# Performance work log

Measured on AMD Instinct MI355X. Metric: run time of the kernel, lower is better.

Reference implementation:

```python
import jax, jax.numpy as jnp
import numpy as np

H = 256  # hidden_dim


def _mlp(x, w1, b1, w2, b2):
    # Linear -> ReLU -> (Dropout=identity in eval) -> Linear
    return jax.nn.relu(x @ w1 + b1) @ w2 + b2


def setup_inputs() -> dict:
    key = jax.random.key(0)
    ks = jax.random.split(key, 9)
    bsz, seq = 32, 4096
    s = 1.0 / np.sqrt(2 * H)
    inp = {
        "h": jax.random.normal(ks[0], (bsz, seq, H), dtype=jnp.float32),
        "mask": jnp.ones((bsz, seq), dtype=jnp.float32),
        "ew1": jax.random.uniform(ks[1], (2 * H, H), minval=-s, maxval=s),
        "eb1": jax.random.uniform(ks[2], (H,), minval=-s, maxval=s),
        "ew2": jax.random.uniform(ks[3], (H, H), minval=-s, maxval=s),
        "eb2": jax.random.uniform(ks[4], (H,), minval=-s, maxval=s),
        "nw1": jax.random.uniform(ks[5], (2 * H, H), minval=-s, maxval=s),
        "nb1": jax.random.uniform(ks[6], (H,), minval=-s, maxval=s),
        "nw2": jax.random.uniform(ks[7], (H, H), minval=-s, maxval=s),
        "nb2": jax.random.uniform(ks[8], (H,), minval=-s, maxval=s),
    }
    return inp


def reference(h, mask, ew1, eb1, ew2, eb2, nw1, nb1, nw2, nb2):
    left = h[:, :-1, :]   # [B, S-1, H]
    right = h[:, 1:, :]   # [B, S-1, H]
    m_lr = _mlp(jnp.concatenate([left, right], axis=-1), ew1, eb1, ew2, eb2)
    m_rl = _mlp(jnp.concatenate([right, left], axis=-1), ew1, eb1, ew2, eb2)
    # shifted scatter-add: agg[:,1:] += m_lr ; agg[:,:-1] += m_rl
    zcol = jnp.zeros_like(h[:, :1, :])
    agg = jnp.concatenate([zcol, m_lr], axis=1) + jnp.concatenate([m_rl, zcol], axis=1)
    updated = _mlp(jnp.concatenate([h, agg], axis=-1), nw1, nb1, nw2, nb2)
    updated = updated * mask[:, :, None]
    return h + updated
```

## Files before the change

### kernel.cpp

```cpp
#include <hip/hip_runtime.h>
#include <hip/hip_bf16.h>

typedef __bf16 bf16_t;
typedef bf16_t bf16x8 __attribute__((ext_vector_type(8)));
typedef bf16_t bf16x4 __attribute__((ext_vector_type(4)));
typedef float f32x4 __attribute__((ext_vector_type(4)));

#define SEQ 4096
#define BSZ 32
#define T_TOK 96
#define TILES 43
#define PROWS 98
#define LSTR 264
#define NPANEL (PROWS * LSTR)

#define OFF_X 0
#define OFF_A NPANEL
#define OFF_B (2 * NPANEL)
#define SMEM_ELEMS (3 * NPANEL)
#define SMEM_BYTES (SMEM_ELEMS * 2)

#define W1F 0
#define NAF 131072
#define WBF 196608
#define N2F 262144
#define B2N 327680

#define BAR() asm volatile("s_waitcnt lgkmcnt(0)\n\ts_barrier" ::: "memory")

__global__ void wprep(const float* __restrict__ ew1, const float* __restrict__ nw1,
                      const float* __restrict__ nw2, bf16_t* __restrict__ wsw) {
    int idx = blockIdx.x * 256 + threadIdx.x;
    int region, rel, outbase;
    if (idx < 131072)      { region = 0; rel = idx;          outbase = W1F; }
    else if (idx < 196608) { region = 1; rel = idx - 131072; outbase = NAF; }
    else                   { region = 2; rel = idx - 196608; outbase = N2F; }
    int f = rel >> 9, o = rel & 511;
    int l = o >> 3, e = o & 7;
    int r = l & 15, kg = l >> 4;
    int nt = f >> 3, ks = f & 7;
    int k = ks * 32 + kg * 8 + e;
    int n = nt * 16 + r;
    float v;
    if (region == 0)
        v = (nt < 16) ? ew1[k * 256 + n] : ew1[(256 + k) * 256 + (n - 256)];
    else if (region == 1)
        v = nw1[k * 256 + n];
    else
        v = nw2[k * 256 + n];
    wsw[outbase + rel] = (bf16_t)v;
}

__global__ void wprep2(const float* __restrict__ ew2, const float* __restrict__ eb2,
                       const float* __restrict__ nw1, bf16_t* __restrict__ wsw) {
    int k = blockIdx.x;
    int n = threadIdx.x;
    if (k < 256) {
        float acc = 0.f;
        for (int j = 0; j < 256; ++j)
            acc += ew2[k * 256 + j] * nw1[(256 + j) * 256 + n];
        int ks = k >> 5, kg = (k >> 3) & 3, e = k & 7;
        int nt = n >> 4, r = n & 15;
        wsw[WBF + ((nt * 8 + ks) << 9) + ((kg * 16 + r) << 3) + e] = (bf16_t)acc;
    } else {
        float acc = 0.f;
        for (int j = 0; j < 256; ++j)
            acc += eb2[j] * nw1[(256 + j) * 256 + n];
        ((float*)(wsw + B2N))[n] = acc;
    }
}

__launch_bounds__(512, 2)
__global__ void gnl_kernel(const float* __restrict__ h, const float* __restrict__ mask,
                           const float* __restrict__ eb1, const float* __restrict__ nb1,
                           const float* __restrict__ nb2,
                           const bf16_t* __restrict__ wsw, float* __restrict__ out) {
    extern __shared__ bf16_t sm[];

    const int tid   = threadIdx.x;
    const int lane  = tid & 63;
    const int w     = tid >> 6;
    const int batch = blockIdx.x / TILES;
    const int tile  = blockIdx.x % TILES;
    const int t0    = tile * T_TOK;
    const long baseTok = (long)batch * SEQ;

    const int c   = lane & 15;
    const int kg  = lane >> 4;
    const int crb = kg << 2;
    const int n0a = w * 16;
    const int n0b = (w + 8) * 16;

    auto loadw = [&](bf16x8 (&f)[8], int base, int nt) {
#pragma unroll
        for (int ks = 0; ks < 8; ++ks)
            f[ks] = *(const bf16x8*)(wsw + base + ((nt * 8 + ks) << 9) + (lane << 3));
    };
    auto loada = [&](bf16x8 (&f)[8], int poff, int rbase) {
        const bf16_t* p = sm + poff + (rbase + c) * LSTR + (kg << 3);
#pragma unroll
        for (int ks = 0; ks < 8; ++ks) f[ks] = *(const bf16x8*)(p + (ks << 5));
    };
    auto mfma2 = [&](bf16x8 (&f)[8], bf16x8 (&wa)[8], bf16x8 (&wb)[8],
                     f32x4& a0, f32x4& a1) {
        __builtin_amdgcn_s_setprio(1);
#pragma unroll
        for (int ks = 0; ks < 8; ++ks) {
            a0 = __builtin_amdgcn_mfma_f32_16x16x32_bf16(wa[ks], f[ks], a0, 0, 0, 0);
            a1 = __builtin_amdgcn_mfma_f32_16x16x32_bf16(wb[ks], f[ks], a1, 0, 0, 0);
        }
        __builtin_amdgcn_s_setprio(0);
    };

    bf16x8 wa0[8], wb0[8];
    loadw(wa0, W1F, w);
    loadw(wb0, W1F, w + 8);

#pragma unroll
    for (int it = 0; it < 7; ++it) {
        int cc = tid + it * 512;
        if (cc < PROWS * 32) {
            int r = cc >> 5;
            int fc = (cc & 31) << 3;
            int t = t0 - 1 + r;
            bf16x8 v;
            if (t >= 0 && t < SEQ) {
                const float* src = h + (((long)(baseTok + t)) << 8) + fc;
                float4 x0 = ((const float4*)src)[0];
                float4 x1 = ((const float4*)src)[1];
                v[0] = (bf16_t)x0.x; v[1] = (bf16_t)x0.y;
                v[2] = (bf16_t)x0.z; v[3] = (bf16_t)x0.w;
                v[4] = (bf16_t)x1.x; v[5] = (bf16_t)x1.y;
                v[6] = (bf16_t)x1.z; v[7] = (bf16_t)x1.w;
            } else {
#pragma unroll
                for (int q = 0; q < 8; ++q) v[q] = (bf16_t)0.0f;
            }
            *(bf16x8*)(sm + OFF_X + r * LSTR + fc) = v;
        }
    }
    BAR();

#pragma unroll
    for (int p = 0; p < 2; ++p) {
        bf16x8 wa[8], wb[8];
        if (p == 0) {
#pragma unroll
            for (int ks = 0; ks < 8; ++ks) { wa[ks] = wa0[ks]; wb[ks] = wb0[ks]; }
        } else {
            loadw(wa, W1F, w + 16);
            loadw(wb, W1F, w + 24);
        }
        int poff = p ? OFF_B : OFF_A;
        bf16x8 fA[8], fB[8];
        loada(fA, OFF_X, 0);
#pragma unroll
        for (int mt = 0; mt < 7; ++mt) {
            bf16x8 (&cur)[8] = (mt & 1) ? fB : fA;
            bf16x8 (&nxt)[8] = (mt & 1) ? fA : fB;
            if (mt < 6) loada(nxt, OFF_X, (mt + 1) * 16);
            f32x4 aA = {0.f, 0.f, 0.f, 0.f}, aB = {0.f, 0.f, 0.f, 0.f};
            mfma2(cur, wa, wb, aA, aB);
            int row = mt * 16 + c;
            if (row < PROWS) {
                bf16x4 pA, pB;
#pragma unroll
                for (int q = 0; q < 4; ++q) { pA[q] = (bf16_t)aA[q]; pB[q] = (bf16_t)aB[q]; }
                *(bf16x4*)(sm + poff + row * LSTR + n0a + crb) = pA;
                *(bf16x4*)(sm + poff + row * LSTR + n0b + crb) = pB;
            }
        }
    }

    bf16x8 na[8], nb8[8], wba[8], wbb[8];
    loadw(na, NAF, w);
    loadw(nb8, NAF, w + 8);
    loadw(wba, WBF, w);
    loadw(wbb, WBF, w + 8);
    BAR();

    bf16x8 svr[6];
#pragma unroll
    for (int it = 0; it < 6; ++it) {
        int cc = tid + it * 512;
        int i = cc >> 5;
        int fc = (cc & 31) << 3;
        float bl = (t0 + i >= 1) ? 1.f : 0.f;
        float br = (t0 + i <= SEQ - 2) ? 1.f : 0.f;
        bf16x8 aL = *(const bf16x8*)(sm + OFF_A + i * LSTR + fc);
        bf16x8 aR = *(const bf16x8*)(sm + OFF_A + (i + 2) * LSTR + fc);
        bf16x8 bC = *(const bf16x8*)(sm + OFF_B + (i + 1) * LSTR + fc);
        float4 b1a = *(const float4*)(eb1 + fc);
        float4 b1b = *(const float4*)(eb1 + fc + 4);
        bf16x8 sv;
#pragma unroll
        for (int q = 0; q < 8; ++q) {
            float b1f = (q < 4) ? ((const float*)&b1a)[q] : ((const float*)&b1b)[q - 4];
            float x = (float)bC[q] + b1f;
            float l = fmaxf((float)aL[q] + x, 0.f) * bl;
            float r = fmaxf((float)aR[q] + x, 0.f) * br;
            sv[q] = (bf16_t)(l + r);
        }
        svr[it] = sv;
    }
    BAR();
#pragma unroll
    for (int it = 0; it < 6; ++it) {
        int cc = tid + it * 512;
        int i = cc >> 5;
        int fc = (cc & 31) << 3;
        *(bf16x8*)(sm + OFF_B + i * LSTR + fc) = svr[it];
    }
    BAR();

    {
        float4 n1a = *(const float4*)(nb1 + n0a + crb);
        float4 n1b = *(const float4*)(nb1 + n0b + crb);
        const float* b2n = (const float*)(wsw + B2N);
        float4 c2a = *(const float4*)(b2n + n0a + crb);
        float4 c2b = *(const float4*)(b2n + n0b + crb);
        bf16x8 fX[8], fS[8];
#pragma unroll
        for (int tm = 0; tm < 6; ++tm) {
            loada(fX, OFF_X, 1 + tm * 16);
            loada(fS, OFF_B, tm * 16);
            f32x4 a0 = {0.f, 0.f, 0.f, 0.f}, a1 = {0.f, 0.f, 0.f, 0.f};
            mfma2(fX, na, nb8, a0, a1);
            mfma2(fS, wba, wbb, a0, a1);
            int row = tm * 16 + c;
            int t = t0 + row;
            float cnt = ((t >= 1) ? 1.f : 0.f) + ((t <= SEQ - 2) ? 1.f : 0.f);
            bf16x4 p0, p1;
#pragma unroll
            for (int q = 0; q < 4; ++q) {
                p0[q] = (bf16_t)fmaxf(a0[q] + ((const float*)&n1a)[q] + cnt * ((const float*)&c2a)[q], 0.f);
                p1[q] = (bf16_t)fmaxf(a1[q] + ((const float*)&n1b)[q] + cnt * ((const float*)&c2b)[q], 0.f);
            }
            *(bf16x4*)(sm + OFF_A + row * LSTR + n0a + crb) = p0;
            *(bf16x4*)(sm + OFF_A + row * LSTR + n0b + crb) = p1;
        }
    }
    bf16x8 n2a[8], n2b[8];
    loadw(n2a, N2F, w);
    loadw(n2b, N2F, w + 8);
    BAR();

    {
        float4 v2a = *(const float4*)(nb2 + n0a + crb);
        float4 v2b = *(const float4*)(nb2 + n0b + crb);
        bf16x8 fA[8], fB[8];
        loada(fA, OFF_A, 0);
#pragma unroll
        for (int tm = 0; tm < 6; ++tm) {
            int row = tm * 16 + c;
            int tok = t0 + row;
            int tokc = (tok < SEQ) ? tok : (SEQ - 1);
            long t = baseTok + tokc;
            float m = mask[t];
            bf16x8 (&cur)[8] = (tm & 1) ? fB : fA;
            bf16x8 (&nxt)[8] = (tm & 1) ? fA : fB;
            if (tm < 5) loada(nxt, OFF_A, (tm + 1) * 16);
            f32x4 a0 = {0.f, 0.f, 0.f, 0.f}, a1 = {0.f, 0.f, 0.f, 0.f};
            mfma2(cur, n2a, n2b, a0, a1);
            int rrow = row + 1;
            bf16x4 r0 = *(const bf16x4*)(sm + OFF_X + rrow * LSTR + n0a + crb);
            bf16x4 r1 = *(const bf16x4*)(sm + OFF_X + rrow * LSTR + n0b + crb);
            if (tok < SEQ) {
                long g0 = (t << 8) + n0a + crb;
                long g1 = (t << 8) + n0b + crb;
                float4 o0, o1;
                o0.x = (float)r0[0] + m * (a0[0] + v2a.x);
                o0.y = (float)r0[1] + m * (a0[1] + v2a.y);
                o0.z = (float)r0[2] + m * (a0[2] + v2a.z);
                o0.w = (float)r0[3] + m * (a0[3] + v2a.w);
                o1.x = (float)r1[0] + m * (a1[0] + v2b.x);
                o1.y = (float)r1[1] + m * (a1[1] + v2b.y);
                o1.z = (float)r1[2] + m * (a1[2] + v2b.z);
                o1.w = (float)r1[3] + m * (a1[3] + v2b.w);
                *(float4*)(out + g0) = o0;
                *(float4*)(out + g1) = o1;
            }
        }
    }
}

extern "C" void kernel_launch(void* const* d_in, const int* in_sizes, int n_in,
                              void* d_out, int out_size, void* d_ws, size_t ws_size,
                              hipStream_t stream) {
    const float* h    = (const float*)d_in[0];
    const float* mask = (const float*)d_in[1];
    const float* ew1  = (const float*)d_in[2];
    const float* eb1  = (const float*)d_in[3];
    const float* ew2  = (const float*)d_in[4];
    const float* eb2  = (const float*)d_in[5];
    const float* nw1  = (const float*)d_in[6];
    const float* nb1  = (const float*)d_in[7];
    const float* nw2  = (const float*)d_in[8];
    const float* nb2  = (const float*)d_in[9];
    float* out   = (float*)d_out;
    bf16_t* wsw  = (bf16_t*)d_ws;

    wprep<<<1024, 256, 0, stream>>>(ew1, nw1, nw2, wsw);
    wprep2<<<257, 256, 0, stream>>>(ew2, eb2, nw1, wsw);

    hipFuncSetAttribute(reinterpret_cast<const void*>(gnl_kernel),
                        hipFuncAttributeMaxDynamicSharedMemorySize, SMEM_BYTES);

    gnl_kernel<<<BSZ * TILES, 512, SMEM_BYTES, stream>>>(
        h, mask, eb1, nb1, nb2, wsw, out);
}
```

Measured before the change: 146.8 us.

## Shrink token tile, software-pipeline input load, split node GEMM to cut registers

Reduces the per-block token tile from 96 to 86 (48 tiles per batch), so LDS panels get smaller and more blocks can be resident, with loada clamping rows for the partial last MMA tile. Global loads of h are double-buffered so the next stage's fetch is issued before the current stage is converted and stored. The aggregate computation now writes in place, dropping a barrier and the staging registers. The node layer-1 GEMM is split into two passes with the partial sum kept in LDS, so only one weight set is live at a time. The cost is extra LDS traffic and bf16 rounding of the intermediate partial sum, plus some wasted MMA work on padded rows.

```diff
diff --git a/kernel.cpp b/kernel.cpp
--- a/kernel.cpp
+++ b/kernel.cpp
@@ -8,9 +8,9 @@
 
 #define SEQ 4096
 #define BSZ 32
-#define T_TOK 96
-#define TILES 43
-#define PROWS 98
+#define T_TOK 86
+#define TILES 48
+#define PROWS 88
 #define LSTR 264
 #define NPANEL (PROWS * LSTR)
 
@@ -97,7 +97,9 @@
             f[ks] = *(const bf16x8*)(wsw + base + ((nt * 8 + ks) << 9) + (lane << 3));
     };
     auto loada = [&](bf16x8 (&f)[8], int poff, int rbase) {
-        const bf16_t* p = sm + poff + (rbase + c) * LSTR + (kg << 3);
+        int rr = rbase + c;
+        rr = (rr < PROWS) ? rr : (PROWS - 1);
+        const bf16_t* p = sm + poff + rr * LSTR + (kg << 3);
 #pragma unroll
         for (int ks = 0; ks < 8; ++ks) f[ks] = *(const bf16x8*)(p + (ks << 5));
     };
@@ -116,27 +118,46 @@
     loadw(wa0, W1F, w);
     loadw(wb0, W1F, w + 8);
 
-#pragma unroll
-    for (int it = 0; it < 7; ++it) {
-        int cc = tid + it * 512;
-        if (cc < PROWS * 32) {
-            int r = cc >> 5;
-            int fc = (cc & 31) << 3;
-            int t = t0 - 1 + r;
-            bf16x8 v;
-            if (t >= 0 && t < SEQ) {
-                const float* src = h + (((long)(baseTok + t)) << 8) + fc;
-                float4 x0 = ((const float4*)src)[0];
-                float4 x1 = ((const float4*)src)[1];
-                v[0] = (bf16_t)x0.x; v[1] = (bf16_t)x0.y;
-                v[2] = (bf16_t)x0.z; v[3] = (bf16_t)x0.w;
-                v[4] = (bf16_t)x1.x; v[5] = (bf16_t)x1.y;
-                v[6] = (bf16_t)x1.z; v[7] = (bf16_t)x1.w;
-            } else {
-#pragma unroll
-                for (int q = 0; q < 8; ++q) v[q] = (bf16_t)0.0f;
-            }
-            *(bf16x8*)(sm + OFF_X + r * LSTR + fc) = v;
+    {
+        float4 pa0, pa1, pb0, pb1;
+        auto issue_stage = [&](int it, float4& q0, float4& q1) {
+            int cc = tid + it * 512;
+            if (cc < PROWS * 32) {
+                int r = cc >> 5, fc = (cc & 31) << 3;
+                int t = t0 - 1 + r;
+                int tc = (t < 0) ? 0 : ((t > SEQ - 1) ? SEQ - 1 : t);
+                const float* src = h + (((long)(baseTok + tc)) << 8) + fc;
+                q0 = ((const float4*)src)[0];
+                q1 = ((const float4*)src)[1];
+            }
+        };
+        auto write_stage = [&](int it, const float4& q0, const float4& q1) {
+            int cc = tid + it * 512;
+            if (cc < PROWS * 32) {
+                int r = cc >> 5, fc = (cc & 31) << 3;
+                int t = t0 - 1 + r;
+                bf16x8 v;
+                if (t >= 0 && t < SEQ) {
+                    v[0] = (bf16_t)q0.x; v[1] = (bf16_t)q0.y;
+                    v[2] = (bf16_t)q0.z; v[3] = (bf16_t)q0.w;
+                    v[4] = (bf16_t)q1.x; v[5] = (bf16_t)q1.y;
+                    v[6] = (bf16_t)q1.z; v[7] = (bf16_t)q1.w;
+                } else {
+#pragma unroll
+                    for (int q = 0; q < 8; ++q) v[q] = (bf16_t)0.0f;
+                }
+                *(bf16x8*)(sm + OFF_X + r * LSTR + fc) = v;
+            }
+        };
+        issue_stage(0, pa0, pa1);
+#pragma unroll
+        for (int it = 0; it < 6; ++it) {
+            if (it < 5) {
+                if (it & 1) issue_stage(it + 1, pa0, pa1);
+                else        issue_stage(it + 1, pb0, pb1);
+            }
+            if (it & 1) write_stage(it, pb0, pb1);
+            else        write_stage(it, pa0, pa1);
         }
     }
     BAR();
@@ -155,10 +176,10 @@
         bf16x8 fA[8], fB[8];
         loada(fA, OFF_X, 0);
 #pragma unroll
-        for (int mt = 0; mt < 7; ++mt) {
+        for (int mt = 0; mt < 6; ++mt) {
             bf16x8 (&cur)[8] = (mt & 1) ? fB : fA;
             bf16x8 (&nxt)[8] = (mt & 1) ? fA : fB;
-            if (mt < 6) loada(nxt, OFF_X, (mt + 1) * 16);
+            if (mt < 5) loada(nxt, OFF_X, (mt + 1) * 16);
             f32x4 aA = {0.f, 0.f, 0.f, 0.f}, aB = {0.f, 0.f, 0.f, 0.f};
             mfma2(cur, wa, wb, aA, aB);
             int row = mt * 16 + c;
@@ -172,72 +193,86 @@
         }
     }
 
-    bf16x8 na[8], nb8[8], wba[8], wbb[8];
+    bf16x8 na[8], nb8[8];
     loadw(na, NAF, w);
     loadw(nb8, NAF, w + 8);
-    loadw(wba, WBF, w);
-    loadw(wbb, WBF, w + 8);
     BAR();
 
-    bf16x8 svr[6];
 #pragma unroll
     for (int it = 0; it < 6; ++it) {
         int cc = tid + it * 512;
-        int i = cc >> 5;
-        int fc = (cc & 31) << 3;
-        float bl = (t0 + i >= 1) ? 1.f : 0.f;
-        float br = (t0 + i <= SEQ - 2) ? 1.f : 0.f;
-        bf16x8 aL = *(const bf16x8*)(sm + OFF_A + i * LSTR + fc);
-        bf16x8 aR = *(const bf16x8*)(sm + OFF_A + (i + 2) * LSTR + fc);
-        bf16x8 bC = *(const bf16x8*)(sm + OFF_B + (i + 1) * LSTR + fc);
-        float4 b1a = *(const float4*)(eb1 + fc);
-        float4 b1b = *(const float4*)(eb1 + fc + 4);
-        bf16x8 sv;
-#pragma unroll
-        for (int q = 0; q < 8; ++q) {
-            float b1f = (q < 4) ? ((const float*)&b1a)[q] : ((const float*)&b1b)[q - 4];
-            float x = (float)bC[q] + b1f;
-            float l = fmaxf((float)aL[q] + x, 0.f) * bl;
-            float r = fmaxf((float)aR[q] + x, 0.f) * br;
-            sv[q] = (bf16_t)(l + r);
-        }
-        svr[it] = sv;
+        if (cc < T_TOK * 32) {
+            int i = cc >> 5;
+            int fc = (cc & 31) << 3;
+            float bl = (t0 + i >= 1) ? 1.f : 0.f;
+            float br = (t0 + i <= SEQ - 2) ? 1.f : 0.f;
+            bf16x8 aL = *(const bf16x8*)(sm + OFF_A + i * LSTR + fc);
+            bf16x8 aR = *(const bf16x8*)(sm + OFF_A + (i + 2) * LSTR + fc);
+            bf16x8 bC = *(const bf16x8*)(sm + OFF_B + (i + 1) * LSTR + fc);
+            float4 b1a = *(const float4*)(eb1 + fc);
+            float4 b1b = *(const float4*)(eb1 + fc + 4);
+            bf16x8 sv;
+#pragma unroll
+            for (int q = 0; q < 8; ++q) {
+                float b1f = (q < 4) ? ((const float*)&b1a)[q] : ((const float*)&b1b)[q - 4];
+                float x = (float)bC[q] + b1f;
+                float l = fmaxf((float)aL[q] + x, 0.f) * bl;
+                float r = fmaxf((float)aR[q] + x, 0.f) * br;
+                sv[q] = (bf16_t)(l + r);
+            }
+            *(bf16x8*)(sm + OFF_B + (i + 1) * LSTR + fc) = sv;
+        }
     }
     BAR();
-#pragma unroll
-    for (int it = 0; it < 6; ++it) {
-        int cc = tid + it * 512;
-        int i = cc >> 5;
-        int fc = (cc & 31) << 3;
-        *(bf16x8*)(sm + OFF_B + i * LSTR + fc) = svr[it];
-    }
-    BAR();
 
     {
+        bf16x8 fX[8];
+#pragma unroll
+        for (int tm = 0; tm < 6; ++tm) {
+            loada(fX, OFF_X, 1 + tm * 16);
+            f32x4 a0 = {0.f, 0.f, 0.f, 0.f}, a1 = {0.f, 0.f, 0.f, 0.f};
+            mfma2(fX, na, nb8, a0, a1);
+            int row = tm * 16 + c;
+            if (row < T_TOK) {
+                bf16x4 p0, p1;
+#pragma unroll
+                for (int q = 0; q < 4; ++q) { p0[q] = (bf16_t)a0[q]; p1[q] = (bf16_t)a1[q]; }
+                *(bf16x4*)(sm + OFF_A + row * LSTR + n0a + crb) = p0;
+                *(bf16x4*)(sm + OFF_A + row * LSTR + n0b + crb) = p1;
+            }
+        }
+    }
+
+    {
+        bf16x8 wba[8], wbb[8];
+        loadw(wba, WBF, w);
+        loadw(wbb, WBF, w + 8);
         float4 n1a = *(const float4*)(nb1 + n0a + crb);
         float4 n1b = *(const float4*)(nb1 + n0b + crb);
         const float* b2n = (const float*)(wsw + B2N);
         float4 c2a = *(const float4*)(b2n + n0a + crb);
         float4 c2b = *(const float4*)(b2n + n0b + crb);
-        bf16x8 fX[8], fS[8];
+        bf16x8 fS[8];
 #pragma unroll
         for (int tm = 0; tm < 6; ++tm) {
-            loada(fX, OFF_X, 1 + tm * 16);
-            loada(fS, OFF_B, tm * 16);
+            loada(fS, OFF_B, 1 + tm * 16);
             f32x4 a0 = {0.f, 0.f, 0.f, 0.f}, a1 = {0.f, 0.f, 0.f, 0.f};
-            mfma2(fX, na, nb8, a0, a1);
             mfma2(fS, wba, wbb, a0, a1);
             int row = tm * 16 + c;
-            int t = t0 + row;
-            float cnt = ((t >= 1) ? 1.f : 0.f) + ((t <= SEQ - 2) ? 1.f : 0.f);
-            bf16x4 p0, p1;
-#pragma unroll
-            for (int q = 0; q < 4; ++q) {
-                p0[q] = (bf16_t)fmaxf(a0[q] + ((const float*)&n1a)[q] + cnt * ((const float*)&c2a)[q], 0.f);
-                p1[q] = (bf16_t)fmaxf(a1[q] + ((const float*)&n1b)[q] + cnt * ((const float*)&c2b)[q], 0.f);
-            }
-            *(bf16x4*)(sm + OFF_A + row * LSTR + n0a + crb) = p0;
-            *(bf16x4*)(sm + OFF_A + row * LSTR + n0b + crb) = p1;
+            if (row < T_TOK) {
+                bf16x4 q0 = *(const bf16x4*)(sm + OFF_A + row * LSTR + n0a + crb);
+                bf16x4 q1 = *(const bf16x4*)(sm + OFF_A + row * LSTR + n0b + crb);
+                int t = t0 + row;
+                float cnt = ((t >= 1) ? 1.f : 0.f) + ((t <= SEQ - 2) ? 1.f : 0.f);
+                bf16x4 p0, p1;
+#pragma unroll
+                for (int q = 0; q < 4; ++q) {
+                    p0[q] = (bf16_t)fmaxf(a0[q] + (float)q0[q] + ((const float*)&n1a)[q] + cnt * ((const float*)&c2a)[q], 0.f);
+                    p1[q] = (bf16_t)fmaxf(a1[q] + (float)q1[q] + ((const float*)&n1b)[q] + cnt * ((const float*)&c2b)[q], 0.f);
+                }
+                *(bf16x4*)(sm + OFF_A + row * LSTR + n0a + crb) = p0;
+                *(bf16x4*)(sm + OFF_A + row * LSTR + n0b + crb) = p1;
+            }
         }
     }
     bf16x8 n2a[8], n2b[8];
@@ -263,9 +298,10 @@
             f32x4 a0 = {0.f, 0.f, 0.f, 0.f}, a1 = {0.f, 0.f, 0.f, 0.f};
             mfma2(cur, n2a, n2b, a0, a1);
             int rrow = row + 1;
+            rrow = (rrow < PROWS) ? rrow : (PROWS - 1);
             bf16x4 r0 = *(const bf16x4*)(sm + OFF_X + rrow * LSTR + n0a + crb);
             bf16x4 r1 = *(const bf16x4*)(sm + OFF_X + rrow * LSTR + n0b + crb);
-            if (tok < SEQ) {
+            if (row < T_TOK && tok < SEQ) {
                 long g0 = (t << 8) + n0a + crb;
                 long g1 = (t << 8) + n0b + crb;
                 float4 o0, o1;
```

Measured after the change: 150.8 us. 2.7% more time.

## Overlap second half of input load with first GEMM pass; in-place edge combine

Applied to the files above, without the earlier changes.

The input tile load is split. The first 64 rows are converted and stored, and the remaining rows' global loads are issued into registers before the first-pass MFMA on those 64 rows runs, which hides global latency behind compute. The edge-combine step now writes each result back in place, shifted by one row, which removes a register staging array and one barrier. The shifted offset is carried into the next GEMM's loads. The cost is extra registers held across the MFMA phase and one additional barrier in the load phase.

```diff
diff --git a/kernel.cpp b/kernel.cpp
--- a/kernel.cpp
+++ b/kernel.cpp
@@ -117,21 +117,71 @@
     loadw(wb0, W1F, w + 8);
 
 #pragma unroll
-    for (int it = 0; it < 7; ++it) {
+    for (int it = 0; it < 4; ++it) {
         int cc = tid + it * 512;
+        int r = cc >> 5;
+        int fc = (cc & 31) << 3;
+        int t = t0 - 1 + r;
+        bf16x8 v;
+        if (t >= 0 && t < SEQ) {
+            const float* src = h + (((long)(baseTok + t)) << 8) + fc;
+            float4 x0 = ((const float4*)src)[0];
+            float4 x1 = ((const float4*)src)[1];
+            v[0] = (bf16_t)x0.x; v[1] = (bf16_t)x0.y;
+            v[2] = (bf16_t)x0.z; v[3] = (bf16_t)x0.w;
+            v[4] = (bf16_t)x1.x; v[5] = (bf16_t)x1.y;
+            v[6] = (bf16_t)x1.z; v[7] = (bf16_t)x1.w;
+        } else {
+#pragma unroll
+            for (int q = 0; q < 8; ++q) v[q] = (bf16_t)0.0f;
+        }
+        *(bf16x8*)(sm + OFF_X + r * LSTR + fc) = v;
+    }
+    float4 s0[3], s1[3];
+#pragma unroll
+    for (int k = 0; k < 3; ++k) {
+        int cc = tid + (k + 4) * 512;
         if (cc < PROWS * 32) {
-            int r = cc >> 5;
-            int fc = (cc & 31) << 3;
+            int r = cc >> 5, fc = (cc & 31) << 3;
+            int t = t0 - 1 + r;
+            int tc = (t > SEQ - 1) ? SEQ - 1 : t;
+            const float* src = h + (((long)(baseTok + tc)) << 8) + fc;
+            s0[k] = ((const float4*)src)[0];
+            s1[k] = ((const float4*)src)[1];
+        }
+    }
+    BAR();
+
+    {
+        bf16x8 fA[8], fB[8];
+        loada(fA, OFF_X, 0);
+#pragma unroll
+        for (int mt = 0; mt < 4; ++mt) {
+            bf16x8 (&cur)[8] = (mt & 1) ? fB : fA;
+            bf16x8 (&nxt)[8] = (mt & 1) ? fA : fB;
+            if (mt < 3) loada(nxt, OFF_X, (mt + 1) * 16);
+            f32x4 aA = {0.f, 0.f, 0.f, 0.f}, aB = {0.f, 0.f, 0.f, 0.f};
+            mfma2(cur, wa0, wb0, aA, aB);
+            int row = mt * 16 + c;
+            bf16x4 pA, pB;
+#pragma unroll
+            for (int q = 0; q < 4; ++q) { pA[q] = (bf16_t)aA[q]; pB[q] = (bf16_t)aB[q]; }
+            *(bf16x4*)(sm + OFF_A + row * LSTR + n0a + crb) = pA;
+            *(bf16x4*)(sm + OFF_A + row * LSTR + n0b + crb) = pB;
+        }
+    }
+#pragma unroll
+    for (int k = 0; k < 3; ++k) {
+        int cc = tid + (k + 4) * 512;
+        if (cc < PROWS * 32) {
+            int r = cc >> 5, fc = (cc & 31) << 3;
             int t = t0 - 1 + r;
             bf16x8 v;
-            if (t >= 0 && t < SEQ) {
-                const float* src = h + (((long)(baseTok + t)) << 8) + fc;
-                float4 x0 = ((const float4*)src)[0];
-                float4 x1 = ((const float4*)src)[1];
-                v[0] = (bf16_t)x0.x; v[1] = (bf16_t)x0.y;
-                v[2] = (bf16_t)x0.z; v[3] = (bf16_t)x0.w;
-                v[4] = (bf16_t)x1.x; v[5] = (bf16_t)x1.y;
-                v[6] = (bf16_t)x1.z; v[7] = (bf16_t)x1.w;
+            if (t < SEQ) {
+                v[0] = (bf16_t)s0[k].x; v[1] = (bf16_t)s0[k].y;
+                v[2] = (bf16_t)s0[k].z; v[3] = (bf16_t)s0[k].w;
+                v[4] = (bf16_t)s1[k].x; v[5] = (bf16_t)s1[k].y;
+                v[6] = (bf16_t)s1[k].z; v[7] = (bf16_t)s1[k].w;
             } else {
 #pragma unroll
                 for (int q = 0; q < 8; ++q) v[q] = (bf16_t)0.0f;
@@ -141,17 +191,30 @@
     }
     BAR();
 
-#pragma unroll
-    for (int p = 0; p < 2; ++p) {
+    {
+        bf16x8 fA[8], fB[8];
+        loada(fA, OFF_X, 64);
+#pragma unroll
+        for (int mt = 4; mt < 7; ++mt) {
+            bf16x8 (&cur)[8] = (mt & 1) ? fB : fA;
+            bf16x8 (&nxt)[8] = (mt & 1) ? fA : fB;
+            if (mt < 6) loada(nxt, OFF_X, (mt + 1) * 16);
+            f32x4 aA = {0.f, 0.f, 0.f, 0.f}, aB = {0.f, 0.f, 0.f, 0.f};
+            mfma2(cur, wa0, wb0, aA, aB);
+            int row = mt * 16 + c;
+            if (row < PROWS) {
+                bf16x4 pA, pB;
+#pragma unroll
+                for (int q = 0; q < 4; ++q) { pA[q] = (bf16_t)aA[q]; pB[q] = (bf16_t)aB[q]; }
+                *(bf16x4*)(sm + OFF_A + row * LSTR + n0a + crb) = pA;
+                *(bf16x4*)(sm + OFF_A + row * LSTR + n0b + crb) = pB;
+            }
+        }
+    }
+    {
         bf16x8 wa[8], wb[8];
-        if (p == 0) {
-#pragma unroll
-            for (int ks = 0; ks < 8; ++ks) { wa[ks] = wa0[ks]; wb[ks] = wb0[ks]; }
-        } else {
-            loadw(wa, W1F, w + 16);
-            loadw(wb, W1F, w + 24);
-        }
-        int poff = p ? OFF_B : OFF_A;
+        loadw(wa, W1F, w + 16);
+        loadw(wb, W1F, w + 24);
         bf16x8 fA[8], fB[8];
         loada(fA, OFF_X, 0);
 #pragma unroll
@@ -166,8 +229,8 @@
                 bf16x4 pA, pB;
 #pragma unroll
                 for (int q = 0; q < 4; ++q) { pA[q] = (bf16_t)aA[q]; pB[q] = (bf16_t)aB[q]; }
-                *(bf16x4*)(sm + poff + row * LSTR + n0a + crb) = pA;
-                *(bf16x4*)(sm + poff + row * LSTR + n0b + crb) = pB;
+                *(bf16x4*)(sm + OFF_B + row * LSTR + n0a + crb) = pA;
+                *(bf16x4*)(sm + OFF_B + row * LSTR + n0b + crb) = pB;
             }
         }
     }
@@ -179,7 +242,6 @@
     loadw(wbb, WBF, w + 8);
     BAR();
 
-    bf16x8 svr[6];
 #pragma unroll
     for (int it = 0; it < 6; ++it) {
         int cc = tid + it * 512;
@@ -201,15 +263,7 @@
             float r = fmaxf((float)aR[q] + x, 0.f) * br;
             sv[q] = (bf16_t)(l + r);
         }
-        svr[it] = sv;
-    }
-    BAR();
-#pragma unroll
-    for (int it = 0; it < 6; ++it) {
-        int cc = tid + it * 512;
-        int i = cc >> 5;
-        int fc = (cc & 31) << 3;
-        *(bf16x8*)(sm + OFF_B + i * LSTR + fc) = svr[it];
+        *(bf16x8*)(sm + OFF_B + (i + 1) * LSTR + fc) = sv;
     }
     BAR();
 
@@ -223,7 +277,7 @@
 #pragma unroll
         for (int tm = 0; tm < 6; ++tm) {
             loada(fX, OFF_X, 1 + tm * 16);
-            loada(fS, OFF_B, tm * 16);
+            loada(fS, OFF_B, 1 + tm * 16);
             f32x4 a0 = {0.f, 0.f, 0.f, 0.f}, a1 = {0.f, 0.f, 0.f, 0.f};
             mfma2(fX, na, nb8, a0, a1);
             mfma2(fS, wba, wbb, a0, a1);
```

Result: slower. 174.6 us (+18.9%).
